# Kernel optimization log

Measured on AMD Instinct MI355X. Metric: run time of the kernel, lower is better.

## Reference

```python
import jax, jax.numpy as jnp
import numpy as np

B_SZ, SEQ, D_IN = 8, 4096, 1024
STATE, HEADS = 1024, 16
HEAD_DIM = STATE // HEADS
LN_EPS = 1e-5


def setup_inputs() -> dict:
    key = jax.random.key(0)
    ks = jax.random.split(key, 10)
    inp = {
        "x": jax.random.normal(ks[0], (B_SZ, SEQ, D_IN), dtype=jnp.float32),
        "W_in": jax.random.normal(ks[1], (STATE, D_IN), dtype=jnp.float32) * (1.0 / np.sqrt(D_IN)),
        "b_in": jnp.zeros((STATE,), dtype=jnp.float32),
        "log_A": jax.random.normal(ks[2], (HEADS, HEAD_DIM), dtype=jnp.float32) * 0.1 + 0.1,
        "B_p": jax.random.normal(ks[3], (HEADS, HEAD_DIM), dtype=jnp.float32) * 0.1 + 0.1,
        "C_p": jax.random.normal(ks[4], (HEADS, HEAD_DIM), dtype=jnp.float32) * 0.1 + 0.1,
        "W_out": jax.random.normal(ks[5], (STATE, STATE), dtype=jnp.float32) * (1.0 / np.sqrt(STATE)),
        "b_out": jnp.zeros((STATE,), dtype=jnp.float32),
        "gamma": jnp.ones((STATE,), dtype=jnp.float32),
        "beta": jnp.zeros((STATE,), dtype=jnp.float32),
    }
    return inp


def reference(x, W_in, b_in, log_A, B_p, C_p, W_out, b_out, gamma, beta):
    Bsz, S, _ = x.shape
    H, Dh = log_A.shape
    # input projection: (B,S,state)
    h = jnp.einsum("bsd,ed->bse", x, W_in) + b_in
    h = h.reshape(Bsz, S, H, Dh)
    decay = jnp.exp(-jax.nn.softplus(log_A))  # (H,Dh), time-invariant

    def step(s, xt):  # s,xt: (B,H,Dh)
        s = s * decay + B_p * xt
        return s, C_p * s

    s0 = jnp.zeros((Bsz, H, Dh), dtype=h.dtype)
    _, ys = jax.lax.scan(step, s0, jnp.swapaxes(h, 0, 1))  # ys: (S,B,H,Dh)
    y = jnp.swapaxes(ys, 0, 1).reshape(Bsz, S, H * Dh)
    out = jnp.einsum("bse,fe->bsf", y, W_out) + b_out
    # dropout in eval mode = identity; layer norm over last dim
    mu = out.mean(-1, keepdims=True)
    var = out.var(-1, keepdims=True)
    return (out - mu) * jax.lax.rsqrt(var + LN_EPS) * gamma + beta
```

## Files before the change

### kernel.cpp

```cpp
#include <hip/hip_runtime.h>

#define B_SZ  8
#define SEQ   4096
#define D_IN  1024
#define STATE 1024
#define M_TOT (B_SZ * SEQ)
#define LN_EPS 1e-5f
#define GK    1024
#define GN    1024

#define SCAN_L 128
#define SCAN_W 64

typedef short short8_t __attribute__((ext_vector_type(8)));
typedef float f32x4 __attribute__((ext_vector_type(4)));

__device__ __forceinline__ unsigned short f2bf(float f) {
  union { float f; unsigned u; } v; v.f = f;
  unsigned r = v.u + 0x7fffu + ((v.u >> 16) & 1u);
  return (unsigned short)(r >> 16);
}
__device__ __forceinline__ float bf2f(unsigned short h) {
  union { unsigned u; float f; } v; v.u = ((unsigned)h) << 16;
  return v.f;
}

__device__ __forceinline__ void gload16(const void* g, void* l) {
  __builtin_amdgcn_global_load_lds(
      (const __attribute__((address_space(1))) void*)g,
      (__attribute__((address_space(3))) void*)l, 16, 0, 0);
}

#define BAR()    __builtin_amdgcn_s_barrier()
#define SCHED0() __builtin_amdgcn_sched_barrier(0)

__global__ __launch_bounds__(256) void cast_kernel(const float* __restrict__ in,
                                                   unsigned short* __restrict__ out,
                                                   int n4) {
  int i = blockIdx.x * 256 + threadIdx.x;
  if (i < n4) {
    float4 v = ((const float4*)in)[i];
    ushort4 o;
    o.x = f2bf(v.x); o.y = f2bf(v.y); o.z = f2bf(v.z); o.w = f2bf(v.w);
    ((ushort4*)out)[i] = o;
  }
}


__device__ __forceinline__ void stage(const char* gbase, char* dbase, int t, int q) {
  gload16(gbase + (q * 131072 + t * 128), dbase + q * 8192);
}

template <int H>
__device__ __forceinline__ void readA(const char* pk0, const char* pk1,
                                      short8_t (&a)[4][2]) {
#pragma unroll
  for (int mf = 0; mf < 4; mf++) {
    a[mf][0] = *(const short8_t*)(pk0 + ((H * 64 + mf * 16) << 7));
    a[mf][1] = *(const short8_t*)(pk1 + ((H * 64 + mf * 16) << 7));
  }
}
template <int NH>
__device__ __forceinline__ void readB(const char* pk0, const char* pk1,
                                      short8_t (&b)[2][2]) {
#pragma unroll
  for (int nf = 0; nf < 2; nf++) {
    b[nf][0] = *(const short8_t*)(pk0 + ((NH * 32 + nf * 16) << 7));
    b[nf][1] = *(const short8_t*)(pk1 + ((NH * 32 + nf * 16) << 7));
  }
}

template <int H, int NH>
__device__ __forceinline__ void mfma16(short8_t (&a)[4][2], short8_t (&b)[2][2],
                                       f32x4 (&acc)[8][4]) {
  __builtin_amdgcn_s_setprio(1);
#pragma unroll
  for (int ks = 0; ks < 2; ks++)
#pragma unroll
    for (int mf = 0; mf < 4; mf++)
#pragma unroll
      for (int nf = 0; nf < 2; nf++)
        acc[H * 4 + mf][NH * 2 + nf] = __builtin_amdgcn_mfma_f32_16x16x32_bf16(
            a[mf][ks], b[nf][ks], acc[H * 4 + mf][NH * 2 + nf], 0, 0, 0);
  __builtin_amdgcn_s_setprio(0);
}

__global__ __launch_bounds__(512, 2) void gemm256(
    const unsigned short* __restrict__ A,
    const unsigned short* __restrict__ Bt,
    const float* __restrict__ bias,
    unsigned short* __restrict__ C,
    int M) {
  __shared__ __attribute__((aligned(16))) unsigned short As[2][256 * 64];
  __shared__ __attribute__((aligned(16))) unsigned short Bs[2][256 * 64];

  const int tid = threadIdx.x;
  const int w = tid >> 6, lane = tid & 63;
  const int wm = w >> 2, wn = w & 3;
  const int fr = lane & 15;
  const int fkb = (lane >> 4) * 16;

  const int nwg = gridDim.x;
  const int cpx = nwg >> 3;
  const int bid = blockIdx.x;
  const int wg = (bid & 7) * cpx + (bid >> 3);
  const int nbx = GN >> 8;
  const long m0 = (long)(wg / nbx) * 256;
  const long n0 = (long)(wg % nbx) * 256;

  const int xorv = (fr & 7) << 4;
  const int lo0 = (fr * 128 + 0  + fkb) ^ xorv;
  const int lo1 = (fr * 128 + 64 + fkb) ^ xorv;
  const char* pA0k0 = (const char*)&As[0][0] + wm * 16384 + lo0;
  const char* pA0k1 = (const char*)&As[0][0] + wm * 16384 + lo1;
  const char* pA1k0 = (const char*)&As[1][0] + wm * 16384 + lo0;
  const char* pA1k1 = (const char*)&As[1][0] + wm * 16384 + lo1;
  const char* pB0k0 = (const char*)&Bs[0][0] + wn * 8192 + lo0;
  const char* pB0k1 = (const char*)&Bs[0][0] + wn * 8192 + lo1;
  const char* pB1k0 = (const char*)&Bs[1][0] + wn * 8192 + lo0;
  const char* pB1k1 = (const char*)&Bs[1][0] + wn * 8192 + lo1;

  const int srow = tid >> 3;
  const int c2 = ((tid & 7) * 16) ^ ((srow & 7) << 4);
  const char* gA0 = (const char*)(A  + (m0 + srow) * (long)GK) + c2;
  const char* gB0 = (const char*)(Bt + (n0 + srow) * (long)GK) + c2;
  char* dA0 = (char*)&As[0][0] + ((tid >> 6) << 10);
  char* dA1 = (char*)&As[1][0] + ((tid >> 6) << 10);
  char* dB0 = (char*)&Bs[0][0] + ((tid >> 6) << 10);
  char* dB1 = (char*)&Bs[1][0] + ((tid >> 6) << 10);

  short8_t aE[4][2], aO[4][2], b0[2][2], b1[2][2];
  f32x4 acc[8][4] = {};

  const int nit = (GK >> 6) >> 1;

#pragma unroll
  for (int q = 0; q < 4; q++) stage(gA0, dA0, 0, q);
#pragma unroll
  for (int q = 0; q < 4; q++) stage(gB0, dB0, 0, q);
  stage(gA0, dA1, 1, 0);
  stage(gA0, dA1, 1, 1);
  SCHED0();
  asm volatile("s_waitcnt vmcnt(2)" ::: "memory");
  BAR();

#pragma unroll 1
  for (int i = 0; i < nit; ++i) {
    const bool last = (i == nit - 1);
    const int t1 = 2 * i + 1, t2 = 2 * i + 2, t3 = 2 * i + 3;

    readA<0>(pA0k0, pA0k1, aE);
    readB<0>(pB0k0, pB0k1, b0);
    stage(gA0, dA1, t1, 2);
    stage(gA0, dA1, t1, 3);
    SCHED0(); BAR();
    mfma16<0, 0>(aE, b0, acc);
    SCHED0(); BAR();

    readB<1>(pB0k0, pB0k1, b1);
    stage(gB0, dB1, t1, 0);
    stage(gB0, dB1, t1, 1);
    SCHED0(); BAR();
    mfma16<0, 1>(aE, b1, acc);
    SCHED0(); BAR();

    readA<1>(pA0k0, pA0k1, aO);
    stage(gB0, dB1, t1, 2);
    stage(gB0, dB1, t1, 3);
    SCHED0(); BAR();
    mfma16<1, 0>(aO, b0, acc);
    SCHED0(); BAR();

    if (!last) {
      stage(gA0, dA0, t2, 0);
      stage(gA0, dA0, t2, 1);
    }
    SCHED0(); BAR();
    mfma16<1, 1>(aO, b1, acc);
    SCHED0();
    if (last) { asm volatile("s_waitcnt vmcnt(0)" ::: "memory"); }
    else      { asm volatile("s_waitcnt vmcnt(2)" ::: "memory"); }
    BAR();

    readA<0>(pA1k0, pA1k1, aE);
    readB<0>(pB1k0, pB1k1, b0);
    if (!last) {
      stage(gA0, dA0, t2, 2);
      stage(gA0, dA0, t2, 3);
    }
    SCHED0(); BAR();
    mfma16<0, 0>(aE, b0, acc);
    SCHED0(); BAR();

    readB<1>(pB1k0, pB1k1, b1);
    if (!last) {
      stage(gB0, dB0, t2, 0);
      stage(gB0, dB0, t2, 1);
    }
    SCHED0(); BAR();
    mfma16<0, 1>(aE, b1, acc);
    SCHED0(); BAR();

    readA<1>(pA1k0, pA1k1, aO);
    if (!last) {
      stage(gB0, dB0, t2, 2);
      stage(gB0, dB0, t2, 3);
    }
    SCHED0(); BAR();
    mfma16<1, 0>(aO, b0, acc);
    SCHED0(); BAR();

    if (!last) {
      stage(gA0, dA1, t3, 0);
      stage(gA0, dA1, t3, 1);
    }
    SCHED0(); BAR();
    mfma16<1, 1>(aO, b1, acc);
    SCHED0();
    if (!last) { asm volatile("s_waitcnt vmcnt(2)" ::: "memory"); }
    BAR();
  }

  const int cc = lane & 15;
  const int cr = (lane >> 4) * 4;
  char* epi = (w < 4) ? ((char*)&As[0][0] + w * 16384)
                      : ((char*)&Bs[0][0] + (w - 4) * 16384);
  float bv[4];
#pragma unroll
  for (int nf = 0; nf < 4; nf++) bv[nf] = bias[n0 + wn * 64 + nf * 16 + cc];
#pragma unroll
  for (int mf = 0; mf < 8; mf++) {
#pragma unroll
    for (int r = 0; r < 4; r++) {
      const int row = mf * 16 + cr + r;
      const int rx = (row & 7) << 4;
#pragma unroll
      for (int nf = 0; nf < 4; nf++) {
        const int off = (row * 128 + (nf * 16 + cc) * 2) ^ rx;
        *(unsigned short*)(epi + off) = f2bf(acc[mf][nf][r] + bv[nf]);
      }
    }
  }
  const int rr = lane >> 3;
  const int rdoff = (lane * 16) ^ ((rr & 7) << 4);
  char* cbase = (char*)C + (m0 + wm * 128) * (GN * 2) + n0 * 2 + wn * 128 + (lane & 7) * 16;
#pragma unroll
  for (int s = 0; s < 16; s++) {
    short8_t vv = *(const short8_t*)(epi + s * 1024 + rdoff);
    *(short8_t*)(cbase + (long)(s * 8 + rr) * (GN * 2)) = vv;
  }
}

__global__ __launch_bounds__(256) void scan_kernel(
    const unsigned short* __restrict__ h,
    const float* __restrict__ log_A,
    const float* __restrict__ Bp,
    const float* __restrict__ Cp,
    unsigned short* __restrict__ y) {
  const int e = blockIdx.x * 256 + threadIdx.x;
  const int chunk = blockIdx.y;
  const int b = blockIdx.z;
  const float la = log_A[e];
  const float d = expf(-log1pf(expf(la)));
  const float bp = Bp[e];
  const float cp = Cp[e];
  const long base = ((long)b * SEQ) * STATE + e;
  const int t0 = chunk * SCAN_L;
  const int tw = (t0 >= SCAN_W) ? (t0 - SCAN_W) : 0;
  float s = 0.f;
  for (int t = tw; t < t0; ++t)
    s = fmaf(s, d, bp * bf2f(h[base + (long)t * STATE]));
  for (int t = t0; t < t0 + SCAN_L; ++t) {
    s = fmaf(s, d, bp * bf2f(h[base + (long)t * STATE]));
    y[base + (long)t * STATE] = f2bf(cp * s);
  }
}

__global__ __launch_bounds__(256) void ln_kernel(
    const unsigned short* __restrict__ X,
    const float* __restrict__ gamma,
    const float* __restrict__ beta,
    float* __restrict__ out) {
  const int row = blockIdx.x;
  const int tid = threadIdx.x;
  const long base = (long)row * STATE;
  ushort4 v = *(const ushort4*)&X[base + tid * 4];
  float x0 = bf2f(v.x), x1 = bf2f(v.y), x2 = bf2f(v.z), x3 = bf2f(v.w);
  float s = x0 + x1 + x2 + x3;
  float q = x0 * x0 + x1 * x1 + x2 * x2 + x3 * x3;
#pragma unroll
  for (int o = 32; o > 0; o >>= 1) {
    s += __shfl_xor(s, o);
    q += __shfl_xor(q, o);
  }
  __shared__ float sw[4], qw[4];
  const int wave = tid >> 6, lane = tid & 63;
  if (lane == 0) { sw[wave] = s; qw[wave] = q; }
  __syncthreads();
  s = sw[0] + sw[1] + sw[2] + sw[3];
  q = qw[0] + qw[1] + qw[2] + qw[3];
  const float mu = s * (1.0f / STATE);
  const float var = q * (1.0f / STATE) - mu * mu;
  const float inv = rsqrtf(var + LN_EPS);
  const int c = tid * 4;
  float4 o;
  o.x = (x0 - mu) * inv * gamma[c + 0] + beta[c + 0];
  o.y = (x1 - mu) * inv * gamma[c + 1] + beta[c + 1];
  o.z = (x2 - mu) * inv * gamma[c + 2] + beta[c + 2];
  o.w = (x3 - mu) * inv * gamma[c + 3] + beta[c + 3];
  *(float4*)&out[base + tid * 4] = o;
}

extern "C" void kernel_launch(void* const* d_in, const int* in_sizes, int n_in,
                              void* d_out, int out_size, void* d_ws, size_t ws_size,
                              hipStream_t stream) {
  const float* x     = (const float*)d_in[0];
  const float* W_in  = (const float*)d_in[1];
  const float* b_in  = (const float*)d_in[2];
  const float* log_A = (const float*)d_in[3];
  const float* Bp    = (const float*)d_in[4];
  const float* Cp    = (const float*)d_in[5];
  const float* W_out = (const float*)d_in[6];
  const float* b_out = (const float*)d_in[7];
  const float* gamma = (const float*)d_in[8];
  const float* beta  = (const float*)d_in[9];
  float* out = (float*)d_out;

  char* ws = (char*)d_ws;
  unsigned short* Wi_b = (unsigned short*)(ws);
  unsigned short* Wo_b = (unsigned short*)(ws + (2ull << 20));
  unsigned short* xb   = (unsigned short*)(ws + (4ull << 20));
  unsigned short* hb   = (unsigned short*)(ws + (68ull << 20));

  cast_kernel<<<(M_TOT * D_IN / 4) / 256, 256, 0, stream>>>(x, xb, M_TOT * D_IN / 4);
  cast_kernel<<<(STATE * D_IN / 4) / 256, 256, 0, stream>>>(W_in, Wi_b, STATE * D_IN / 4);
  cast_kernel<<<(STATE * STATE / 4) / 256, 256, 0, stream>>>(W_out, Wo_b, STATE * STATE / 4);

  gemm256<<<dim3((GN / 256) * (M_TOT / 256)), 512, 0, stream>>>(
      xb, Wi_b, b_in, hb, M_TOT);

  scan_kernel<<<dim3(STATE / 256, SEQ / SCAN_L, B_SZ), 256, 0, stream>>>(
      hb, log_A, Bp, Cp, xb);

  gemm256<<<dim3((GN / 256) * (M_TOT / 256)), 512, 0, stream>>>(
      xb, Wo_b, b_out, hb, M_TOT);

  ln_kernel<<<M_TOT, 256, 0, stream>>>(hb, gamma, beta, out);
}
```

Measured before the change: 259.2 us.

## Vectorize scan and layernorm, grid-stride cast kernel, halve scan chunk length

The scan kernel now has each thread handle four contiguous state channels with ushort4 loads and stores, and one block covers the whole state width. Scan chunks shrink from 128 to 64 steps with the same 64-step warmup, so there are more blocks but a larger share of redundant warmup work. The layernorm uses 128 threads with 8-element vector loads and vectorized gamma/beta reads. The cast kernel becomes a grid-stride loop with a fixed grid size.

```diff
diff --git a/kernel.cpp b/kernel.cpp
--- a/kernel.cpp
+++ b/kernel.cpp
@@ -9,7 +9,7 @@
 #define GK    1024
 #define GN    1024
 
-#define SCAN_L 128
+#define SCAN_L 64
 #define SCAN_W 64
 
 typedef short short8_t __attribute__((ext_vector_type(8)));
@@ -37,15 +37,14 @@
 __global__ __launch_bounds__(256) void cast_kernel(const float* __restrict__ in,
                                                    unsigned short* __restrict__ out,
                                                    int n4) {
-  int i = blockIdx.x * 256 + threadIdx.x;
-  if (i < n4) {
+  const int stride = gridDim.x * 256;
+  for (int i = blockIdx.x * 256 + threadIdx.x; i < n4; i += stride) {
     float4 v = ((const float4*)in)[i];
     ushort4 o;
     o.x = f2bf(v.x); o.y = f2bf(v.y); o.z = f2bf(v.z); o.w = f2bf(v.w);
     ((ushort4*)out)[i] = o;
   }
 }
-
 
 __device__ __forceinline__ void stage(const char* gbase, char* dbase, int t, int q) {
   gload16(gbase + (q * 131072 + t * 128), dbase + q * 8192);
@@ -257,26 +256,44 @@
     const float* __restrict__ Bp,
     const float* __restrict__ Cp,
     unsigned short* __restrict__ y) {
-  const int e = blockIdx.x * 256 + threadIdx.x;
-  const int chunk = blockIdx.y;
-  const int b = blockIdx.z;
-  const float la = log_A[e];
-  const float d = expf(-log1pf(expf(la)));
-  const float bp = Bp[e];
-  const float cp = Cp[e];
-  const long base = ((long)b * SEQ) * STATE + e;
+  const int e0 = threadIdx.x * 4;
+  const int chunk = blockIdx.x;
+  const int b = blockIdx.y;
+  const float4 la = *(const float4*)&log_A[e0];
+  const float4 bp = *(const float4*)&Bp[e0];
+  const float4 cp = *(const float4*)&Cp[e0];
+  float d[4], bpv[4], cpv[4];
+  d[0] = expf(-log1pf(expf(la.x))); d[1] = expf(-log1pf(expf(la.y)));
+  d[2] = expf(-log1pf(expf(la.z))); d[3] = expf(-log1pf(expf(la.w)));
+  bpv[0] = bp.x; bpv[1] = bp.y; bpv[2] = bp.z; bpv[3] = bp.w;
+  cpv[0] = cp.x; cpv[1] = cp.y; cpv[2] = cp.z; cpv[3] = cp.w;
+
+  const long base = ((long)b * SEQ) * STATE + e0;
   const int t0 = chunk * SCAN_L;
   const int tw = (t0 >= SCAN_W) ? (t0 - SCAN_W) : 0;
-  float s = 0.f;
-  for (int t = tw; t < t0; ++t)
-    s = fmaf(s, d, bp * bf2f(h[base + (long)t * STATE]));
+  float s[4] = {0.f, 0.f, 0.f, 0.f};
+
+  for (int t = tw; t < t0; ++t) {
+    ushort4 hv = *(const ushort4*)&h[base + (long)t * STATE];
+    s[0] = fmaf(s[0], d[0], bpv[0] * bf2f(hv.x));
+    s[1] = fmaf(s[1], d[1], bpv[1] * bf2f(hv.y));
+    s[2] = fmaf(s[2], d[2], bpv[2] * bf2f(hv.z));
+    s[3] = fmaf(s[3], d[3], bpv[3] * bf2f(hv.w));
+  }
   for (int t = t0; t < t0 + SCAN_L; ++t) {
-    s = fmaf(s, d, bp * bf2f(h[base + (long)t * STATE]));
-    y[base + (long)t * STATE] = f2bf(cp * s);
-  }
-}
-
-__global__ __launch_bounds__(256) void ln_kernel(
+    ushort4 hv = *(const ushort4*)&h[base + (long)t * STATE];
+    s[0] = fmaf(s[0], d[0], bpv[0] * bf2f(hv.x));
+    s[1] = fmaf(s[1], d[1], bpv[1] * bf2f(hv.y));
+    s[2] = fmaf(s[2], d[2], bpv[2] * bf2f(hv.z));
+    s[3] = fmaf(s[3], d[3], bpv[3] * bf2f(hv.w));
+    ushort4 o;
+    o.x = f2bf(cpv[0] * s[0]); o.y = f2bf(cpv[1] * s[1]);
+    o.z = f2bf(cpv[2] * s[2]); o.w = f2bf(cpv[3] * s[3]);
+    *(ushort4*)&y[base + (long)t * STATE] = o;
+  }
+}
+
+__global__ __launch_bounds__(128) void ln_kernel(
     const unsigned short* __restrict__ X,
     const float* __restrict__ gamma,
     const float* __restrict__ beta,
@@ -284,31 +301,41 @@
   const int row = blockIdx.x;
   const int tid = threadIdx.x;
   const long base = (long)row * STATE;
-  ushort4 v = *(const ushort4*)&X[base + tid * 4];
-  float x0 = bf2f(v.x), x1 = bf2f(v.y), x2 = bf2f(v.z), x3 = bf2f(v.w);
-  float s = x0 + x1 + x2 + x3;
-  float q = x0 * x0 + x1 * x1 + x2 * x2 + x3 * x3;
+  short8_t v = *(const short8_t*)&X[base + tid * 8];
+  float x[8];
+#pragma unroll
+  for (int j = 0; j < 8; j++) x[j] = bf2f((unsigned short)v[j]);
+  float s = 0.f, q = 0.f;
+#pragma unroll
+  for (int j = 0; j < 8; j++) { s += x[j]; q += x[j] * x[j]; }
 #pragma unroll
   for (int o = 32; o > 0; o >>= 1) {
     s += __shfl_xor(s, o);
     q += __shfl_xor(q, o);
   }
-  __shared__ float sw[4], qw[4];
+  __shared__ float sw[2], qw[2];
   const int wave = tid >> 6, lane = tid & 63;
   if (lane == 0) { sw[wave] = s; qw[wave] = q; }
   __syncthreads();
-  s = sw[0] + sw[1] + sw[2] + sw[3];
-  q = qw[0] + qw[1] + qw[2] + qw[3];
+  s = sw[0] + sw[1];
+  q = qw[0] + qw[1];
   const float mu = s * (1.0f / STATE);
   const float var = q * (1.0f / STATE) - mu * mu;
   const float inv = rsqrtf(var + LN_EPS);
-  const int c = tid * 4;
-  float4 o;
-  o.x = (x0 - mu) * inv * gamma[c + 0] + beta[c + 0];
-  o.y = (x1 - mu) * inv * gamma[c + 1] + beta[c + 1];
-  o.z = (x2 - mu) * inv * gamma[c + 2] + beta[c + 2];
-  o.w = (x3 - mu) * inv * gamma[c + 3] + beta[c + 3];
-  *(float4*)&out[base + tid * 4] = o;
+  const int c = tid * 8;
+  float4 g0 = *(const float4*)&gamma[c], g1 = *(const float4*)&gamma[c + 4];
+  float4 be0 = *(const float4*)&beta[c], be1 = *(const float4*)&beta[c + 4];
+  float4 o0, o1;
+  o0.x = (x[0] - mu) * inv * g0.x + be0.x;
+  o0.y = (x[1] - mu) * inv * g0.y + be0.y;
+  o0.z = (x[2] - mu) * inv * g0.z + be0.z;
+  o0.w = (x[3] - mu) * inv * g0.w + be0.w;
+  o1.x = (x[4] - mu) * inv * g1.x + be1.x;
+  o1.y = (x[5] - mu) * inv * g1.y + be1.y;
+  o1.z = (x[6] - mu) * inv * g1.z + be1.z;
+  o1.w = (x[7] - mu) * inv * g1.w + be1.w;
+  *(float4*)&out[base + c] = o0;
+  *(float4*)&out[base + c + 4] = o1;
 }
 
 extern "C" void kernel_launch(void* const* d_in, const int* in_sizes, int n_in,
@@ -332,18 +359,18 @@
   unsigned short* xb   = (unsigned short*)(ws + (4ull << 20));
   unsigned short* hb   = (unsigned short*)(ws + (68ull << 20));
 
-  cast_kernel<<<(M_TOT * D_IN / 4) / 256, 256, 0, stream>>>(x, xb, M_TOT * D_IN / 4);
-  cast_kernel<<<(STATE * D_IN / 4) / 256, 256, 0, stream>>>(W_in, Wi_b, STATE * D_IN / 4);
-  cast_kernel<<<(STATE * STATE / 4) / 256, 256, 0, stream>>>(W_out, Wo_b, STATE * STATE / 4);
+  cast_kernel<<<4096, 256, 0, stream>>>(x, xb, M_TOT * D_IN / 4);
+  cast_kernel<<<1024, 256, 0, stream>>>(W_in, Wi_b, STATE * D_IN / 4);
+  cast_kernel<<<1024, 256, 0, stream>>>(W_out, Wo_b, STATE * STATE / 4);
 
   gemm256<<<dim3((GN / 256) * (M_TOT / 256)), 512, 0, stream>>>(
       xb, Wi_b, b_in, hb, M_TOT);
 
-  scan_kernel<<<dim3(STATE / 256, SEQ / SCAN_L, B_SZ), 256, 0, stream>>>(
+  scan_kernel<<<dim3(SEQ / SCAN_L, B_SZ), 256, 0, stream>>>(
       hb, log_A, Bp, Cp, xb);
 
   gemm256<<<dim3((GN / 256) * (M_TOT / 256)), 512, 0, stream>>>(
       xb, Wo_b, b_out, hb, M_TOT);
 
-  ln_kernel<<<M_TOT, 256, 0, stream>>>(hb, gamma, beta, out);
-}
+  ln_kernel<<<M_TOT, 128, 0, stream>>>(hb, gamma, beta, out);
+}
```

Result: no change. 257.1 us (-0.8%).
